# Kernel optimization log

Hardware: AMD Instinct MI355X
Metric: run time of the kernel (lower is better)

The kernel has to match this reference:

```python
import jax, jax.numpy as jnp
import numpy as np

N_NODES = 100000
N_EDGES = 800000
DIM = 300
N_GRAPHS = 64
ATOM_VOCAB = 41
WORD_VOCAB = 10000


def setup_inputs() -> dict:
    key = jax.random.key(0)
    ks = jax.random.split(key, 7)
    atoms = jax.random.randint(ks[0], (N_NODES,), 0, ATOM_VOCAB)
    words = jax.random.randint(ks[1], (N_NODES,), 0, WORD_VOCAB)
    x = jnp.stack([atoms, words], axis=-1)  # [N,2] int indices
    edge_index = jax.random.randint(ks[2], (2, N_EDGES), 0, N_NODES)
    batch = jnp.sort(jax.random.randint(ks[3], (N_NODES,), 0, N_GRAPHS))
    atom_table = jax.random.normal(ks[4], (ATOM_VOCAB, DIM), dtype=jnp.float32) * 0.02
    word_table = jax.random.normal(ks[5], (WORD_VOCAB, DIM), dtype=jnp.float32) * 0.02
    W = jax.random.normal(ks[6], (DIM, DIM), dtype=jnp.float32) / np.sqrt(DIM)
    b = jnp.zeros((DIM,), dtype=jnp.float32)
    return {"x": x, "edge_index": edge_index, "batch": batch,
            "atom_table": atom_table, "word_table": word_table,
            "W": W, "b": b, "num_hops": 3}


def reference(x, edge_index, batch, atom_table, word_table, W, b, num_hops):
    n = x.shape[0]
    # GCNConv: add self-loops, symmetric degree normalization
    loops = jnp.arange(n)
    src = jnp.concatenate([edge_index[0], loops])  # [E+N]
    dst = jnp.concatenate([edge_index[1], loops])
    deg = jax.ops.segment_sum(jnp.ones_like(dst, dtype=W.dtype), dst, num_segments=n)
    dinv = jnp.where(deg > 0, jax.lax.rsqrt(deg), 0.0)
    norm = dinv[src] * dinv[dst]  # [E+N]

    # embed_nodes: atom embedding + word embedding
    h = atom_table[x[:, 0]] + word_table[x[:, 1]]  # [N, D]

    # num_hops applications of the SAME GCNConv (shared W, b)
    for _ in range(num_hops):
        hw = h @ W  # [N, D]
        msg = hw[src] * norm[:, None]  # [E+N, D]
        h = jax.ops.segment_sum(msg, dst, num_segments=n) + b

    # global_mean_pool over batch assignment
    sums = jax.ops.segment_sum(h, batch, num_segments=N_GRAPHS)  # [G, D]
    cnt = jax.ops.segment_sum(jnp.ones((n,), h.dtype), batch, num_segments=N_GRAPHS)
    return sums / jnp.maximum(cnt, 1.0)[:, None]
```

## Files before the change

kernel.cpp:

```cpp
#include <hip/hip_runtime.h>
#include <hip/hip_fp16.h>

#define NG 64
#define NGRAPH_C 64

#define RSZ 25000
#define RSZP4 6250
#define NC_MS 128
#define NRNG 4
#define MSB 1024

#define VOC 10000
#define KPAD 10240
#define NKC 80
#define WGK 128

#define NATOM 41
#define NC_A 128
#define ASL 128
#define TW_BLKS ((VOC + 3) / 4)
#define TA_BLKS ((NATOM * ASL + 3) / 4)

__device__ __forceinline__ unsigned f_as_u(float f) { union { float f; unsigned u; } c; c.f = f; return c.u; }
__device__ __forceinline__ float u_as_f(unsigned u) { union { unsigned u; float f; } c; c.u = u; return c.f; }

__device__ __forceinline__ int xcc_id() {
    unsigned x;
    asm volatile("s_getreg_b32 %0, hwreg(HW_REG_XCC_ID)" : "=s"(x));
    return (int)(x & 7u);
}

union H4 { uint2 u2; __half h[4]; };

__global__ __launch_bounds__(MSB) void k_mscount(const int* __restrict__ src, const int* __restrict__ dst,
                                                 unsigned* __restrict__ rep_in,
                                                 unsigned* __restrict__ rep_src,
                                                 int e, int n, int chunk, int nwords) {
    __shared__ unsigned hin[RSZP4];
    __shared__ unsigned hsrc[RSZP4];
    int c = blockIdx.x % NC_MS;
    int r = blockIdx.x / NC_MS;
    int base = r * RSZ;
    int t = threadIdx.x;
    for (int w = t; w < RSZP4; w += MSB) { hin[w] = 0u; hsrc[w] = 0u; }
    __syncthreads();
    int e0 = c * chunk, e1 = min(e, e0 + chunk);
    for (int i = e0 + t; i < e1; i += MSB) {
        int s = src[i], d = dst[i];
        unsigned ud = (unsigned)(d - base);
        unsigned us = (unsigned)(s - base);
        if (ud < (unsigned)RSZ) atomicAdd(&hin[ud >> 2], 1u << ((ud & 3) * 8));
        if (us < (unsigned)RSZ) atomicAdd(&hsrc[us >> 2], 1u << ((us & 3) * 8));
    }
    __syncthreads();
    int lim = min(RSZ, n - base);
    if (lim <= 0) return;
    int plim = (lim + 3) >> 2;
    unsigned* gin  = rep_in  + (size_t)c * nwords + (base >> 2);
    unsigned* gsrc = rep_src + (size_t)c * nwords + (base >> 2);
    for (int w = t; w < plim; w += MSB) { gin[w] = hin[w]; gsrc[w] = hsrc[w]; }
}

__global__ __launch_bounds__(256) void k_msreduce(const unsigned* __restrict__ rep_in,
                                                  unsigned* __restrict__ rep_src,
                                                  float* __restrict__ dinv,
                                                  unsigned* __restrict__ counts_src,
                                                  int n, int nwords) {
    int i4 = blockIdx.x * 256 + threadIdx.x;
    if (i4 >= nwords) return;
    unsigned s0 = 0, s1 = 0, s2 = 0, s3 = 0;
    unsigned r0 = 0, r1 = 0, r2 = 0, r3 = 0;
#pragma unroll 4
    for (int c = 0; c < NC_MS; ++c) {
        unsigned vi = rep_in[(size_t)c * nwords + i4];
        s0 += vi & 0xFFu; s1 += (vi >> 8) & 0xFFu; s2 += (vi >> 16) & 0xFFu; s3 += vi >> 24;
        unsigned vs = rep_src[(size_t)c * nwords + i4];
        rep_src[(size_t)c * nwords + i4] = r0 | (r1 << 8) | (r2 << 16) | (r3 << 24);
        r0 += vs & 0xFFu; r1 += (vs >> 8) & 0xFFu; r2 += (vs >> 16) & 0xFFu; r3 += vs >> 24;
    }
    int i = i4 * 4;
    unsigned sv[4] = {s0, s1, s2, s3};
    unsigned rv[4] = {r0, r1, r2, r3};
#pragma unroll
    for (int q = 0; q < 4; ++q) {
        if (i + q < n) {
            dinv[i + q] = rsqrtf((float)(sv[q] + 1u));
            counts_src[i + q] = rv[q];
        }
    }
}

__global__ __launch_bounds__(256) void k_blocksum(const unsigned* __restrict__ counts,
                                                  unsigned* __restrict__ partials, int n) {
    __shared__ unsigned s[256];
    int base = blockIdx.x * 1024;
    unsigned sum = 0;
    for (int j = threadIdx.x; j < 1024; j += 256) {
        int i = base + j;
        sum += (i < n) ? counts[i] : 0u;
    }
    s[threadIdx.x] = sum;
    __syncthreads();
    for (int off = 128; off > 0; off >>= 1) {
        if (threadIdx.x < (unsigned)off) s[threadIdx.x] += s[threadIdx.x + off];
        __syncthreads();
    }
    if (threadIdx.x == 0) partials[blockIdx.x] = s[0];
}

__global__ __launch_bounds__(128) void k_scanpartials(unsigned* __restrict__ partials, int nb) {
    __shared__ unsigned s[128];
    int t = threadIdx.x;
    s[t] = (t < nb) ? partials[t] : 0u;
    __syncthreads();
    if (t == 0) {
        unsigned run = 0;
        for (int i = 0; i < nb; ++i) { unsigned v = s[i]; s[i] = run; run += v; }
    }
    __syncthreads();
    if (t < nb) partials[t] = s[t];
}

__global__ __launch_bounds__(256) void k_scanblock(const unsigned* __restrict__ counts,
                                                   const unsigned* __restrict__ partials,
                                                   unsigned* __restrict__ row_start, int n) {
    __shared__ unsigned s[256];
    int base = blockIdx.x * 1024;
    int t = threadIdx.x;
    unsigned v[4];
    unsigned tsum = 0;
#pragma unroll
    for (int j = 0; j < 4; ++j) {
        int i = base + t * 4 + j;
        v[j] = (i < n) ? counts[i] : 0u;
        tsum += v[j];
    }
    s[t] = tsum;
    __syncthreads();
    for (int off = 1; off < 256; off <<= 1) {
        unsigned x = (t >= off) ? s[t - off] : 0u;
        __syncthreads();
        s[t] += x;
        __syncthreads();
    }
    unsigned excl = (t > 0 ? s[t - 1] : 0u) + partials[blockIdx.x];
#pragma unroll
    for (int j = 0; j < 4; ++j) {
        int i = base + t * 4 + j;
        if (i < n) {
            row_start[i] = excl;
            excl += v[j];
            if (i == n - 1) row_start[n] = excl;
        }
    }
}

__global__ __launch_bounds__(MSB) void k_msfill(const int* __restrict__ src, const int* __restrict__ dst,
                                                const int* __restrict__ batch,
                                                const unsigned* __restrict__ row_start,
                                                const unsigned* __restrict__ pref,
                                                const float* __restrict__ dinv,
                                                uint2* __restrict__ euv,
                                                int e, int n, int chunk, int nwords) {
    __shared__ unsigned cur[RSZP4];
    int c = blockIdx.x % NC_MS;
    int r = blockIdx.x / NC_MS;
    int base = r * RSZ;
    int t = threadIdx.x;
    for (int w = t; w < RSZP4; w += MSB) cur[w] = 0u;
    __syncthreads();
    int e0 = c * chunk, e1 = min(e, e0 + chunk);
    const unsigned* prefc = pref + (size_t)c * nwords;
    for (int i = e0 + t; i < e1; i += MSB) {
        int s = src[i];
        unsigned us = (unsigned)(s - base);
        if (us < (unsigned)RSZ) {
            int d = dst[i];
            unsigned sh = (us & 3) * 8;
            unsigned old = atomicAdd(&cur[us >> 2], 1u << sh);
            unsigned slot = (old >> sh) & 0xFFu;
            unsigned p8 = (prefc[(unsigned)s >> 2] >> ((s & 3) * 8)) & 0xFFu;
            unsigned pos = row_start[s] + p8 + slot;
            uint2 pv;
            pv.x = (unsigned)d | ((unsigned)batch[d] << 17);
            pv.y = f_as_u(dinv[s] * dinv[d]);
            euv[pos] = pv;
        }
    }
}

__global__ __launch_bounds__(256) void k_xcount(const int* __restrict__ x,
                                                unsigned* __restrict__ wcnt,
                                                unsigned* __restrict__ rep_a,
                                                int n, int chunk) {
    __shared__ unsigned h[NATOM];
    int c = blockIdx.x;
    int t = threadIdx.x;
    if (t < NATOM) h[t] = 0u;
    __syncthreads();
    int j0 = c * chunk, j1 = min(n, j0 + chunk);
    for (int j = j0 + t; j < j1; j += 256) {
        int2 xv = *(const int2*)&x[2 * j];
        atomicAdd(&h[xv.x], 1u);
        atomicAdd(&wcnt[xv.y], 1u);
    }
    __syncthreads();
    if (t < NATOM) rep_a[c * NATOM + t] = h[t];
}

__global__ __launch_bounds__(1024) void k_scanall(const unsigned* __restrict__ wcnt,
                                                  unsigned* __restrict__ wstart,
                                                  unsigned* __restrict__ rep_a,
                                                  unsigned* __restrict__ astart,
                                                  const int* __restrict__ batch,
                                                  int* __restrict__ gstart, int n) {
    __shared__ unsigned s[1024];
    __shared__ unsigned tot[NATOM];
    int t = threadIdx.x;
    if (t < NATOM) {
        unsigned run = 0;
        for (int c = 0; c < NC_A; ++c) {
            unsigned v = rep_a[c * NATOM + t];
            rep_a[c * NATOM + t] = run;
            run += v;
        }
        tot[t] = run;
    }
    if (t <= NGRAPH_C) {
        if (t == NGRAPH_C) gstart[t] = n;
        else {
            int lo = 0, hi = n;
            while (lo < hi) {
                int mid = (lo + hi) >> 1;
                if (batch[mid] < t) lo = mid + 1; else hi = mid;
            }
            gstart[t] = lo;
        }
    }
    int lo10 = t * 10;
    unsigned v[10];
    unsigned sum = 0;
    if (lo10 < VOC) {
#pragma unroll
        for (int q = 0; q < 10; ++q) { v[q] = wcnt[lo10 + q]; sum += v[q]; }
    }
    s[t] = sum;
    __syncthreads();
    for (int off = 1; off < 1024; off <<= 1) {
        unsigned xx = (t >= off) ? s[t - off] : 0u;
        __syncthreads();
        s[t] += xx;
        __syncthreads();
    }
    if (lo10 < VOC) {
        unsigned excl = (t > 0) ? s[t - 1] : 0u;
#pragma unroll
        for (int q = 0; q < 10; ++q) { wstart[lo10 + q] = excl; excl += v[q]; }
    }
    if (t == 1023) wstart[VOC] = s[1023];
    if (t == 0) {
        unsigned run = 0;
        for (int a = 0; a < NATOM; ++a) { astart[a] = run; run += tot[a]; }
        astart[NATOM] = run;
    }
}

__global__ __launch_bounds__(256) void k_xfill(const int* __restrict__ x,
                                               const unsigned* __restrict__ wstart,
                                               unsigned* __restrict__ wcur,
                                               unsigned* __restrict__ sorted,
                                               const unsigned* __restrict__ astart,
                                               const unsigned* __restrict__ rep_a,
                                               unsigned* __restrict__ asorted,
                                               int n, int chunk) {
    __shared__ unsigned cur[NATOM];
    __shared__ unsigned base[NATOM];
    int c = blockIdx.x;
    int t = threadIdx.x;
    if (t < NATOM) {
        cur[t] = 0u;
        base[t] = astart[t] + rep_a[c * NATOM + t];
    }
    __syncthreads();
    int j0 = c * chunk, j1 = min(n, j0 + chunk);
    for (int j = j0 + t; j < j1; j += 256) {
        int2 xv = *(const int2*)&x[2 * j];
        unsigned slot = atomicAdd(&cur[xv.x], 1u);
        asorted[base[xv.x] + slot] = (unsigned)j;
        unsigned pos = wstart[xv.y] + atomicAdd(&wcur[xv.y], 1u);
        sorted[pos] = (unsigned)j;
    }
}

__global__ __launch_bounds__(256) void k_y1(const int* __restrict__ batch,
                                            const float* __restrict__ dinv,
                                            const unsigned* __restrict__ row_start,
                                            const uint2* __restrict__ euv,
                                            __half* __restrict__ Y1, int n) {
    int idx = blockIdx.x * 256 + threadIdx.x;
    if (idx >= n * 16) return;
    int j = idx >> 4;
    int c4 = idx & 15;
    int cb = c4 * 4;
    float a0 = 0.f, a1 = 0.f, a2 = 0.f, a3 = 0.f;
    {
        int bj = batch[j];
        float dj = dinv[j];
        float sn = dj * dj;
        a0 += (bj == cb + 0) ? sn : 0.f;
        a1 += (bj == cb + 1) ? sn : 0.f;
        a2 += (bj == cb + 2) ? sn : 0.f;
        a3 += (bj == cb + 3) ? sn : 0.f;
    }
    unsigned e0 = row_start[j], e1 = row_start[j + 1];
    unsigned e = e0;
    for (; e + 4 <= e1; e += 4) {
        uint2 p0 = euv[e], p1 = euv[e + 1], p2 = euv[e + 2], p3 = euv[e + 3];
        int b0 = (int)(p0.x >> 17), b1 = (int)(p1.x >> 17);
        int b2 = (int)(p2.x >> 17), b3 = (int)(p3.x >> 17);
        float v0 = u_as_f(p0.y), v1 = u_as_f(p1.y);
        float v2 = u_as_f(p2.y), v3 = u_as_f(p3.y);
        a0 += ((b0 == cb + 0) ? v0 : 0.f) + ((b1 == cb + 0) ? v1 : 0.f)
            + ((b2 == cb + 0) ? v2 : 0.f) + ((b3 == cb + 0) ? v3 : 0.f);
        a1 += ((b0 == cb + 1) ? v0 : 0.f) + ((b1 == cb + 1) ? v1 : 0.f)
            + ((b2 == cb + 1) ? v2 : 0.f) + ((b3 == cb + 1) ? v3 : 0.f);
        a2 += ((b0 == cb + 2) ? v0 : 0.f) + ((b1 == cb + 2) ? v1 : 0.f)
            + ((b2 == cb + 2) ? v2 : 0.f) + ((b3 == cb + 2) ? v3 : 0.f);
        a3 += ((b0 == cb + 3) ? v0 : 0.f) + ((b1 == cb + 3) ? v1 : 0.f)
            + ((b2 == cb + 3) ? v2 : 0.f) + ((b3 == cb + 3) ? v3 : 0.f);
    }
    for (; e < e1; ++e) {
        uint2 p = euv[e];
        int bd = (int)(p.x >> 17);
        float v = u_as_f(p.y);
        a0 += (bd == cb + 0) ? v : 0.f;
        a1 += (bd == cb + 1) ? v : 0.f;
        a2 += (bd == cb + 2) ? v : 0.f;
        a3 += (bd == cb + 3) ? v : 0.f;
    }
    H4 o;
    o.h[0] = __float2half(a0); o.h[1] = __float2half(a1);
    o.h[2] = __float2half(a2); o.h[3] = __float2half(a3);
    *(uint2*)&Y1[(size_t)j * NG + cb] = o.u2;
}

__global__ __launch_bounds__(256) void k_yprop(const __half* __restrict__ Yin,
                                               const float* __restrict__ dinv,
                                               const unsigned* __restrict__ row_start,
                                               const uint2* __restrict__ euv,
                                               __half* __restrict__ Yout, int n) {
    int idx = blockIdx.x * 256 + threadIdx.x;
    if (idx >= n * 16) return;
    int j = idx >> 4;
    int c4 = idx & 15;
    int cb = c4 * 4;
    float dj = dinv[j];
    float sn = dj * dj;
    H4 s; s.u2 = *(const uint2*)&Yin[(size_t)j * NG + cb];
    float a0 = sn * __half2float(s.h[0]);
    float a1 = sn * __half2float(s.h[1]);
    float a2 = sn * __half2float(s.h[2]);
    float a3 = sn * __half2float(s.h[3]);
    unsigned e0 = row_start[j], e1 = row_start[j + 1];
    unsigned e = e0;
    for (; e + 4 <= e1; e += 4) {
        uint2 p0 = euv[e], p1 = euv[e + 1], p2 = euv[e + 2], p3 = euv[e + 3];
        float v0 = u_as_f(p0.y), v1 = u_as_f(p1.y);
        float v2 = u_as_f(p2.y), v3 = u_as_f(p3.y);
        H4 m0; m0.u2 = *(const uint2*)&Yin[(size_t)(p0.x & 0x1FFFFu) * NG + cb];
        H4 m1; m1.u2 = *(const uint2*)&Yin[(size_t)(p1.x & 0x1FFFFu) * NG + cb];
        H4 m2; m2.u2 = *(const uint2*)&Yin[(size_t)(p2.x & 0x1FFFFu) * NG + cb];
        H4 m3; m3.u2 = *(const uint2*)&Yin[(size_t)(p3.x & 0x1FFFFu) * NG + cb];
        a0 += v0 * __half2float(m0.h[0]) + v1 * __half2float(m1.h[0])
            + v2 * __half2float(m2.h[0]) + v3 * __half2float(m3.h[0]);
        a1 += v0 * __half2float(m0.h[1]) + v1 * __half2float(m1.h[1])
            + v2 * __half2float(m2.h[1]) + v3 * __half2float(m3.h[1]);
        a2 += v0 * __half2float(m0.h[2]) + v1 * __half2float(m1.h[2])
            + v2 * __half2float(m2.h[2]) + v3 * __half2float(m3.h[2]);
        a3 += v0 * __half2float(m0.h[3]) + v1 * __half2float(m1.h[3])
            + v2 * __half2float(m2.h[3]) + v3 * __half2float(m3.h[3]);
    }
    for (; e < e1; ++e) {
        uint2 p0 = euv[e];
        float v0 = u_as_f(p0.y);
        H4 m0; m0.u2 = *(const uint2*)&Yin[(size_t)(p0.x & 0x1FFFFu) * NG + cb];
        a0 += v0 * __half2float(m0.h[0]);
        a1 += v0 * __half2float(m0.h[1]);
        a2 += v0 * __half2float(m0.h[2]);
        a3 += v0 * __half2float(m0.h[3]);
    }
    H4 o;
    o.h[0] = __float2half(a0); o.h[1] = __float2half(a1);
    o.h[2] = __float2half(a2); o.h[3] = __float2half(a3);
    *(uint2*)&Yout[(size_t)j * NG + cb] = o.u2;
}

__global__ __launch_bounds__(256) void k_colsumh(const __half* __restrict__ Y,
                                                 float* __restrict__ su8, int n) {
    __shared__ float red[16][NG];
    int t = threadIdx.x;
    int cg = t & 15;
    int sr = t >> 4;
    float a0 = 0.f, a1 = 0.f, a2 = 0.f, a3 = 0.f;
    int stride = gridDim.x * 16;
    for (int j = blockIdx.x * 16 + sr; j < n; j += stride) {
        H4 v; v.u2 = *(const uint2*)&Y[(size_t)j * NG + cg * 4];
        a0 += __half2float(v.h[0]);
        a1 += __half2float(v.h[1]);
        a2 += __half2float(v.h[2]);
        a3 += __half2float(v.h[3]);
    }
    red[sr][cg * 4 + 0] = a0;
    red[sr][cg * 4 + 1] = a1;
    red[sr][cg * 4 + 2] = a2;
    red[sr][cg * 4 + 3] = a3;
    __syncthreads();
    if (t < NG) {
        float s = 0.f;
#pragma unroll
        for (int q = 0; q < 16; ++q) s += red[q][t];
        int r = xcc_id();
        __hip_atomic_fetch_add(&su8[r * NG + t], s,
                               __ATOMIC_RELAXED, __HIP_MEMORY_SCOPE_WORKGROUP);
    }
}

__global__ __launch_bounds__(256) void k_twta(const __half* __restrict__ Y3,
                                              const unsigned* __restrict__ sorted,
                                              const unsigned* __restrict__ wstart,
                                              float* __restrict__ tw,
                                              const unsigned* __restrict__ asorted,
                                              const unsigned* __restrict__ astart,
                                              float* __restrict__ tap) {
    int t = threadIdx.x;
    int g = t & 63;
    if (blockIdx.x < TW_BLKS) {
        int w = blockIdx.x * 4 + (t >> 6);
        if (w >= VOC) return;
        unsigned i0 = wstart[w], i1 = wstart[w + 1];
        float s = 0.f;
        unsigned i = i0;
        for (; i + 2 <= i1; i += 2) {
            unsigned j0 = sorted[i], j1 = sorted[i + 1];
            s += __half2float(Y3[(size_t)j0 * NG + g]) + __half2float(Y3[(size_t)j1 * NG + g]);
        }
        if (i < i1) s += __half2float(Y3[(size_t)sorted[i] * NG + g]);
        tw[(size_t)w * NG + g] = s;
    } else {
        int wid = (blockIdx.x - TW_BLKS) * 4 + (t >> 6);
        if (wid >= NATOM * ASL) return;
        int a  = wid >> 7;
        int sl = wid & (ASL - 1);
        unsigned i0 = astart[a], i1 = astart[a + 1];
        unsigned len = i1 - i0;
        unsigned lo = i0 + (unsigned)((unsigned long long)len * sl / ASL);
        unsigned hi = i0 + (unsigned)((unsigned long long)len * (sl + 1) / ASL);
        float s = 0.f;
        unsigned i = lo;
        for (; i + 2 <= hi; i += 2) {
            unsigned j0 = asorted[i], j1 = asorted[i + 1];
            s += __half2float(Y3[(size_t)j0 * NG + g]) + __half2float(Y3[(size_t)j1 * NG + g]);
        }
        if (i < hi) s += __half2float(Y3[(size_t)asorted[i] * NG + g]);
        tap[((size_t)a * ASL + sl) * NG + g] = s;
    }
}

__global__ __launch_bounds__(256) void k_wgemm2(const float* __restrict__ T,
                                                const float* __restrict__ Tab,
                                                float* __restrict__ Gpart,
                                                const float* __restrict__ tap,
                                                float* __restrict__ ta) {
    if (blockIdx.x == 5) {
        int i = blockIdx.y * 256 + threadIdx.x;
        if (i >= NATOM * NG) return;
        int a = i >> 6;
        int g = i & 63;
        float s = 0.f;
        for (int sl = 0; sl < ASL; ++sl) s += tap[((size_t)a * ASL + sl) * NG + g];
        ta[i] = s;
        return;
    }
    __shared__ float Asm[32 * 64];
    __shared__ float Bsm[32 * 64];
    const int t = threadIdx.x;
    const int tg = t >> 4;
    const int tc = t & 15;
    const int c0 = blockIdx.x * 64;
    const int kb = blockIdx.y * WGK;

    float acc[4][4] = {};

    for (int sub = 0; sub < WGK / 32; ++sub) {
        int kbase = kb + sub * 32;
#pragma unroll
        for (int r2 = 0; r2 < 2; ++r2) {
            int idx4 = r2 * 256 + t;
            int k = idx4 >> 4, g4 = idx4 & 15;
            float4 v = *(const float4*)&T[(size_t)(kbase + k) * 64 + g4 * 4];
            *(float4*)&Asm[k * 64 + g4 * 4] = v;
        }
#pragma unroll
        for (int r2 = 0; r2 < 2; ++r2) {
            int idx4 = r2 * 256 + t;
            int k = idx4 >> 4, c4i = idx4 & 15;
            int gk = kbase + k;
            int cb2 = c0 + c4i * 4;
            float4 v;
            if (gk < VOC && cb2 + 3 < 300) {
                v = *(const float4*)&Tab[(size_t)gk * 300 + cb2];
            } else {
                float tmp[4];
#pragma unroll
                for (int q = 0; q < 4; ++q)
                    tmp[q] = (gk < VOC && cb2 + q < 300) ? Tab[(size_t)gk * 300 + cb2 + q] : 0.f;
                v.x = tmp[0]; v.y = tmp[1]; v.z = tmp[2]; v.w = tmp[3];
            }
            *(float4*)&Bsm[k * 64 + c4i * 4] = v;
        }
        __syncthreads();
#pragma unroll 8
        for (int k = 0; k < 32; ++k) {
            float4 a4 = *(const float4*)&Asm[k * 64 + tg * 4];
            float4 b4 = *(const float4*)&Bsm[k * 64 + tc * 4];
            float a[4] = {a4.x, a4.y, a4.z, a4.w};
            float b[4] = {b4.x, b4.y, b4.z, b4.w};
#pragma unroll
            for (int i = 0; i < 4; ++i)
#pragma unroll
                for (int jj = 0; jj < 4; ++jj) acc[i][jj] += a[i] * b[jj];
        }
        __syncthreads();
    }

    float* gp = Gpart + (size_t)blockIdx.y * (NG * 300);
#pragma unroll
    for (int i = 0; i < 4; ++i) {
        int g = tg * 4 + i;
#pragma unroll
        for (int jj = 0; jj < 4; ++jj) {
            int c = c0 + tc * 4 + jj;
            if (c < 300) gp[g * 300 + c] = acc[i][jj];
        }
    }
}

__global__ __launch_bounds__(256) void k_gredagemm(const float* __restrict__ Gpart,
                                                   const float* __restrict__ ta,
                                                   const float* __restrict__ at,
                                                   float* __restrict__ G0) {
    int k = blockIdx.x * 256 + threadIdx.x;
    if (k >= NG * 300) return;
    if (blockIdx.y < 8) {
        int p0 = blockIdx.y * (NKC / 8);
        int p1 = p0 + (NKC / 8);
        float s = 0.f;
        for (int p = p0; p < p1; ++p) s += Gpart[(size_t)p * (NG * 300) + k];
        atomicAdd(&G0[k], s);
    } else {
        int g = k / 300, c = k - g * 300;
        float acc = 0.f;
#pragma unroll
        for (int q = 0; q < NATOM; ++q) acc += ta[q * NG + g] * at[(size_t)q * 300 + c];
        atomicAdd(&G0[k], acc);
    }
}

__global__ __launch_bounds__(256) void k_smm(const float* __restrict__ A,
                                             const float* __restrict__ W,
                                             float* __restrict__ C,
                                             const float* __restrict__ vin,
                                             float* __restrict__ r_out) {
    int bx = blockIdx.x;
    if (bx >= 75) {
        int c = (bx - 75) * 256 + threadIdx.x;
        if (c >= 300) return;
        int k0 = blockIdx.y * 60;
        float acc = 0.f;
        for (int k = k0; k < k0 + 60; ++k) acc += vin[k] * W[k * 300 + c];
        atomicAdd(&r_out[c], acc);
        return;
    }
    int j = bx * 256 + threadIdx.x;
    if (j >= NG * 300) return;
    int g = j / 300, c = j - g * 300;
    int k0 = blockIdx.y * 60;
    float acc = 0.f;
#pragma unroll 1
    for (int k = k0; k < k0 + 60; k += 4) {
        float a0 = A[g * 300 + k + 0], a1 = A[g * 300 + k + 1];
        float a2 = A[g * 300 + k + 2], a3 = A[g * 300 + k + 3];
        float w0 = W[(k + 0) * 300 + c], w1 = W[(k + 1) * 300 + c];
        float w2 = W[(k + 2) * 300 + c], w3 = W[(k + 3) * 300 + c];
        acc += a0 * w0 + a1 * w1 + a2 * w2 + a3 * w3;
    }
    atomicAdd(&C[j], acc);
}

__global__ __launch_bounds__(256) void k_out(const float* __restrict__ T3,
                                             const float* __restrict__ su1,
                                             const float* __restrict__ su2,
                                             const int* __restrict__ gstart,
                                             const float* __restrict__ r1,
                                             const float* __restrict__ r2,
                                             const float* __restrict__ b,
                                             float* __restrict__ out) {
    int j = blockIdx.x * 256 + threadIdx.x;
    if (j >= NG * 300) return;
    int g = j / 300, c = j - g * 300;
    int cnt = gstart[g + 1] - gstart[g];
    float s1 = 0.f, s2 = 0.f;
#pragma unroll
    for (int r = 0; r < 8; ++r) {
        s1 += su1[r * NG + g];
        s2 += su2[r * NG + g];
    }
    float v = T3[j] + s2 * r2[c] + s1 * r1[c] + (float)cnt * b[c];
    out[j] = v / (float)(cnt > 0 ? cnt : 1);
}

extern "C" void kernel_launch(void* const* d_in, const int* in_sizes, int n_in,
                              void* d_out, int out_size, void* d_ws, size_t ws_size,
                              hipStream_t stream) {
    const int*   x     = (const int*)d_in[0];
    const int*   ei    = (const int*)d_in[1];
    const int*   batch = (const int*)d_in[2];
    const float* at    = (const float*)d_in[3];
    const float* wt    = (const float*)d_in[4];
    const float* W     = (const float*)d_in[5];
    const float* b     = (const float*)d_in[6];

    const int n = in_sizes[0] / 2;
    const int e = in_sizes[1] / 2;

    char* ws = (char*)d_ws;
    size_t off = 0;
    auto carve = [&](size_t bytes) {
        void* p = ws + off;
        off += (bytes + 255) & ~(size_t)255;
        return p;
    };
    __half*   Y1        = (__half*)carve((size_t)n * NG * 2);
    __half*   Y2        = (__half*)carve((size_t)n * NG * 2);
    __half*   Y3        = (__half*)carve((size_t)n * NG * 2);
    uint2*    euv       = (uint2*)carve((size_t)e * 8);
    float*    dinv      = (float*)carve((size_t)n * 4);
    unsigned* counts_src= (unsigned*)carve((size_t)n * 4);
    unsigned* row_start = (unsigned*)carve((size_t)(n + 1) * 4);
    unsigned* partials  = (unsigned*)carve(1024 * 4);
    int*      gstart    = (int*)carve(65 * 4);
    unsigned* wstart    = (unsigned*)carve((size_t)(VOC + 1) * 4);
    unsigned* sorted    = (unsigned*)carve((size_t)n * 4);
    unsigned* asorted   = (unsigned*)carve((size_t)n * 4);
    unsigned* astart    = (unsigned*)carve((NATOM + 1) * 4);
    unsigned* rep_a     = (unsigned*)carve((size_t)NC_A * NATOM * 4);
    float*    tap       = (float*)carve((size_t)NATOM * ASL * NG * 4);
    char*     zB0       = (char*)carve(0);
    float*    su1       = (float*)carve((size_t)8 * NG * 4);
    float*    su2       = (float*)carve((size_t)8 * NG * 4);
    float*    ta        = (float*)carve((size_t)NATOM * NG * 4);
    float*    tw        = (float*)carve((size_t)KPAD * NG * 4);
    float*    G0        = (float*)carve((size_t)NG * 300 * 4);
    float*    r1        = (float*)carve(300 * 4);
    float*    r2        = (float*)carve(300 * 4);
    float*    T1        = (float*)carve((size_t)NG * 300 * 4);
    float*    T2        = (float*)carve((size_t)NG * 300 * 4);
    float*    T3        = (float*)carve((size_t)NG * 300 * 4);
    unsigned* wcnt      = (unsigned*)carve((size_t)VOC * 4);
    unsigned* wcur      = (unsigned*)carve((size_t)VOC * 4);
    char*     zB1       = (char*)carve(0);

    const int* src = ei;
    const int* dst = ei + e;

    unsigned* rep_in  = (unsigned*)Y1;
    unsigned* rep_src = (unsigned*)Y2;
    float*    Gpart   = (float*)Y1;

    hipMemsetAsync(zB0, 0, (size_t)(zB1 - zB0), stream);

    const int nwords = (n + 3) / 4;
    const int chunk  = (e + NC_MS - 1) / NC_MS;
    const int achunk = (n + NC_A - 1) / NC_A;

    k_mscount<<<NRNG * NC_MS, MSB, 0, stream>>>(src, dst, rep_in, rep_src, e, n, chunk, nwords);
    k_msreduce<<<(nwords + 255) / 256, 256, 0, stream>>>(rep_in, rep_src, dinv, counts_src, n, nwords);
    int NB = (n + 1023) / 1024;
    k_blocksum<<<NB, 256, 0, stream>>>(counts_src, partials, n);
    k_scanpartials<<<1, 128, 0, stream>>>(partials, NB);
    k_scanblock<<<NB, 256, 0, stream>>>(counts_src, partials, row_start, n);
    k_msfill<<<NRNG * NC_MS, MSB, 0, stream>>>(src, dst, batch, row_start, rep_src, dinv, euv, e, n, chunk, nwords);

    k_xcount<<<NC_A, 256, 0, stream>>>(x, wcnt, rep_a, n, achunk);
    k_scanall<<<1, 1024, 0, stream>>>(wcnt, wstart, rep_a, astart, batch, gstart, n);
    k_xfill<<<NC_A, 256, 0, stream>>>(x, wstart, wcur, sorted, astart, rep_a, asorted, n, achunk);

    int yb = (n * 16 + 255) / 256;
    k_y1<<<yb, 256, 0, stream>>>(batch, dinv, row_start, euv, Y1, n);
    k_colsumh<<<512, 256, 0, stream>>>(Y1, su1, n);
    k_yprop<<<yb, 256, 0, stream>>>(Y1, dinv, row_start, euv, Y2, n);
    k_colsumh<<<512, 256, 0, stream>>>(Y2, su2, n);
    k_yprop<<<yb, 256, 0, stream>>>(Y2, dinv, row_start, euv, Y3, n);

    k_twta<<<TW_BLKS + TA_BLKS, 256, 0, stream>>>(Y3, sorted, wstart, tw, asorted, astart, tap);
    {
        dim3 gw(6, NKC);
        k_wgemm2<<<gw, 256, 0, stream>>>(tw, wt, Gpart, tap, ta);
        dim3 gr((NG * 300 + 255) / 256, 9);
        k_gredagemm<<<gr, 256, 0, stream>>>(Gpart, ta, at, G0);
    }

    {
        dim3 gs1(77, 5);
        k_smm<<<gs1, 256, 0, stream>>>(G0, W, T1, b, r1);
        k_smm<<<gs1, 256, 0, stream>>>(T1, W, T2, r1, r2);
        dim3 gs3(75, 5);
        k_smm<<<gs3, 256, 0, stream>>>(T2, W, T3, r2, r2);
    }

    k_out<<<(NG * 300 + 255) / 256, 256, 0, stream>>>(T3, su1, su2, gstart, r1, r2, b, (float*)d_out);
}
```

Baseline: 297.7 us.

## Fuse column sums into propagation kernels and block partial sums into msreduce

The separate column-sum kernels are removed. The column sums of Y1 and Y2 are now computed inside k_y1 and k_yprop from the fp32 accumulators, using a shared-memory reduction and atomics spread over 32 replicas (XCC id times 4). The k_blocksum pass is folded into k_msreduce, which now writes the per-block partials directly, and the block granularity changes from 1024 to 1024 nodes via nwords/256. This removes three kernel launches and two full re-reads of the fp16 Y matrices. In exchange it adds a __syncthreads and atomics to each propagation block, and sums fp32 values rather than fp16-rounded ones.

```diff
diff --git a/kernel.cpp b/kernel.cpp
--- a/kernel.cpp
+++ b/kernel.cpp
@@ -20,6 +20,8 @@
 #define ASL 128
 #define TW_BLKS ((VOC + 3) / 4)
 #define TA_BLKS ((NATOM * ASL + 3) / 4)
+
+#define NREP 32
 
 __device__ __forceinline__ unsigned f_as_u(float f) { union { float f; unsigned u; } c; c.f = f; return c.u; }
 __device__ __forceinline__ float u_as_f(unsigned u) { union { unsigned u; float f; } c; c.u = u; return c.f; }
@@ -65,47 +67,42 @@
                                                   unsigned* __restrict__ rep_src,
                                                   float* __restrict__ dinv,
                                                   unsigned* __restrict__ counts_src,
+                                                  unsigned* __restrict__ partials,
                                                   int n, int nwords) {
-    int i4 = blockIdx.x * 256 + threadIdx.x;
-    if (i4 >= nwords) return;
-    unsigned s0 = 0, s1 = 0, s2 = 0, s3 = 0;
-    unsigned r0 = 0, r1 = 0, r2 = 0, r3 = 0;
+    __shared__ unsigned sred[256];
+    int t = threadIdx.x;
+    int i4 = blockIdx.x * 256 + t;
+    unsigned mysum = 0;
+    if (i4 < nwords) {
+        unsigned s0 = 0, s1 = 0, s2 = 0, s3 = 0;
+        unsigned r0 = 0, r1 = 0, r2 = 0, r3 = 0;
 #pragma unroll 4
-    for (int c = 0; c < NC_MS; ++c) {
-        unsigned vi = rep_in[(size_t)c * nwords + i4];
-        s0 += vi & 0xFFu; s1 += (vi >> 8) & 0xFFu; s2 += (vi >> 16) & 0xFFu; s3 += vi >> 24;
-        unsigned vs = rep_src[(size_t)c * nwords + i4];
-        rep_src[(size_t)c * nwords + i4] = r0 | (r1 << 8) | (r2 << 16) | (r3 << 24);
-        r0 += vs & 0xFFu; r1 += (vs >> 8) & 0xFFu; r2 += (vs >> 16) & 0xFFu; r3 += vs >> 24;
-    }
-    int i = i4 * 4;
-    unsigned sv[4] = {s0, s1, s2, s3};
-    unsigned rv[4] = {r0, r1, r2, r3};
-#pragma unroll
-    for (int q = 0; q < 4; ++q) {
-        if (i + q < n) {
-            dinv[i + q] = rsqrtf((float)(sv[q] + 1u));
-            counts_src[i + q] = rv[q];
-        }
-    }
-}
-
-__global__ __launch_bounds__(256) void k_blocksum(const unsigned* __restrict__ counts,
-                                                  unsigned* __restrict__ partials, int n) {
-    __shared__ unsigned s[256];
-    int base = blockIdx.x * 1024;
-    unsigned sum = 0;
-    for (int j = threadIdx.x; j < 1024; j += 256) {
-        int i = base + j;
-        sum += (i < n) ? counts[i] : 0u;
-    }
-    s[threadIdx.x] = sum;
+        for (int c = 0; c < NC_MS; ++c) {
+            unsigned vi = rep_in[(size_t)c * nwords + i4];
+            s0 += vi & 0xFFu; s1 += (vi >> 8) & 0xFFu; s2 += (vi >> 16) & 0xFFu; s3 += vi >> 24;
+            unsigned vs = rep_src[(size_t)c * nwords + i4];
+            rep_src[(size_t)c * nwords + i4] = r0 | (r1 << 8) | (r2 << 16) | (r3 << 24);
+            r0 += vs & 0xFFu; r1 += (vs >> 8) & 0xFFu; r2 += (vs >> 16) & 0xFFu; r3 += vs >> 24;
+        }
+        int i = i4 * 4;
+        unsigned sv[4] = {s0, s1, s2, s3};
+        unsigned rv[4] = {r0, r1, r2, r3};
+#pragma unroll
+        for (int q = 0; q < 4; ++q) {
+            if (i + q < n) {
+                dinv[i + q] = rsqrtf((float)(sv[q] + 1u));
+                counts_src[i + q] = rv[q];
+                mysum += rv[q];
+            }
+        }
+    }
+    sred[t] = mysum;
     __syncthreads();
     for (int off = 128; off > 0; off >>= 1) {
-        if (threadIdx.x < (unsigned)off) s[threadIdx.x] += s[threadIdx.x + off];
+        if (t < off) sred[t] += sred[t + off];
         __syncthreads();
     }
-    if (threadIdx.x == 0) partials[blockIdx.x] = s[0];
+    if (t == 0) partials[blockIdx.x] = sred[0];
 }
 
 __global__ __launch_bounds__(128) void k_scanpartials(unsigned* __restrict__ partials, int nb) {
@@ -296,14 +293,16 @@
                                             const float* __restrict__ dinv,
                                             const unsigned* __restrict__ row_start,
                                             const uint2* __restrict__ euv,
-                                            __half* __restrict__ Y1, int n) {
-    int idx = blockIdx.x * 256 + threadIdx.x;
-    if (idx >= n * 16) return;
+                                            __half* __restrict__ Y1,
+                                            float* __restrict__ su32, int n) {
+    __shared__ float red[16][NG];
+    int t = threadIdx.x;
+    int idx = blockIdx.x * 256 + t;
     int j = idx >> 4;
     int c4 = idx & 15;
     int cb = c4 * 4;
     float a0 = 0.f, a1 = 0.f, a2 = 0.f, a3 = 0.f;
-    {
+    if (j < n) {
         int bj = batch[j];
         float dj = dinv[j];
         float sn = dj * dj;
@@ -311,116 +310,120 @@
         a1 += (bj == cb + 1) ? sn : 0.f;
         a2 += (bj == cb + 2) ? sn : 0.f;
         a3 += (bj == cb + 3) ? sn : 0.f;
-    }
-    unsigned e0 = row_start[j], e1 = row_start[j + 1];
-    unsigned e = e0;
-    for (; e + 4 <= e1; e += 4) {
-        uint2 p0 = euv[e], p1 = euv[e + 1], p2 = euv[e + 2], p3 = euv[e + 3];
-        int b0 = (int)(p0.x >> 17), b1 = (int)(p1.x >> 17);
-        int b2 = (int)(p2.x >> 17), b3 = (int)(p3.x >> 17);
-        float v0 = u_as_f(p0.y), v1 = u_as_f(p1.y);
-        float v2 = u_as_f(p2.y), v3 = u_as_f(p3.y);
-        a0 += ((b0 == cb + 0) ? v0 : 0.f) + ((b1 == cb + 0) ? v1 : 0.f)
-            + ((b2 == cb + 0) ? v2 : 0.f) + ((b3 == cb + 0) ? v3 : 0.f);
-        a1 += ((b0 == cb + 1) ? v0 : 0.f) + ((b1 == cb + 1) ? v1 : 0.f)
-            + ((b2 == cb + 1) ? v2 : 0.f) + ((b3 == cb + 1) ? v3 : 0.f);
-        a2 += ((b0 == cb + 2) ? v0 : 0.f) + ((b1 == cb + 2) ? v1 : 0.f)
-            + ((b2 == cb + 2) ? v2 : 0.f) + ((b3 == cb + 2) ? v3 : 0.f);
-        a3 += ((b0 == cb + 3) ? v0 : 0.f) + ((b1 == cb + 3) ? v1 : 0.f)
-            + ((b2 == cb + 3) ? v2 : 0.f) + ((b3 == cb + 3) ? v3 : 0.f);
-    }
-    for (; e < e1; ++e) {
-        uint2 p = euv[e];
-        int bd = (int)(p.x >> 17);
-        float v = u_as_f(p.y);
-        a0 += (bd == cb + 0) ? v : 0.f;
-        a1 += (bd == cb + 1) ? v : 0.f;
-        a2 += (bd == cb + 2) ? v : 0.f;
-        a3 += (bd == cb + 3) ? v : 0.f;
-    }
-    H4 o;
-    o.h[0] = __float2half(a0); o.h[1] = __float2half(a1);
-    o.h[2] = __float2half(a2); o.h[3] = __float2half(a3);
-    *(uint2*)&Y1[(size_t)j * NG + cb] = o.u2;
+        unsigned e0 = row_start[j], e1 = row_start[j + 1];
+        unsigned e = e0;
+        for (; e + 4 <= e1; e += 4) {
+            uint2 p0 = euv[e], p1 = euv[e + 1], p2 = euv[e + 2], p3 = euv[e + 3];
+            int b0 = (int)(p0.x >> 17), b1 = (int)(p1.x >> 17);
+            int b2 = (int)(p2.x >> 17), b3 = (int)(p3.x >> 17);
+            float v0 = u_as_f(p0.y), v1 = u_as_f(p1.y);
+            float v2 = u_as_f(p2.y), v3 = u_as_f(p3.y);
+            a0 += ((b0 == cb + 0) ? v0 : 0.f) + ((b1 == cb + 0) ? v1 : 0.f)
+                + ((b2 == cb + 0) ? v2 : 0.f) + ((b3 == cb + 0) ? v3 : 0.f);
+            a1 += ((b0 == cb + 1) ? v0 : 0.f) + ((b1 == cb + 1) ? v1 : 0.f)
+                + ((b2 == cb + 1) ? v2 : 0.f) + ((b3 == cb + 1) ? v3 : 0.f);
+            a2 += ((b0 == cb + 2) ? v0 : 0.f) + ((b1 == cb + 2) ? v1 : 0.f)
+                + ((b2 == cb + 2) ? v2 : 0.f) + ((b3 == cb + 2) ? v3 : 0.f);
+            a3 += ((b0 == cb + 3) ? v0 : 0.f) + ((b1 == cb + 3) ? v1 : 0.f)
+                + ((b2 == cb + 3) ? v2 : 0.f) + ((b3 == cb + 3) ? v3 : 0.f);
+        }
+        for (; e < e1; ++e) {
+            uint2 p = euv[e];
+            int bd = (int)(p.x >> 17);
+            float v = u_as_f(p.y);
+            a0 += (bd == cb + 0) ? v : 0.f;
+            a1 += (bd == cb + 1) ? v : 0.f;
+            a2 += (bd == cb + 2) ? v : 0.f;
+            a3 += (bd == cb + 3) ? v : 0.f;
+        }
+        H4 o;
+        o.h[0] = __float2half(a0); o.h[1] = __float2half(a1);
+        o.h[2] = __float2half(a2); o.h[3] = __float2half(a3);
+        *(uint2*)&Y1[(size_t)j * NG + cb] = o.u2;
+    }
+    int slot = t >> 4;
+    red[slot][c4 * 4 + 0] = a0;
+    red[slot][c4 * 4 + 1] = a1;
+    red[slot][c4 * 4 + 2] = a2;
+    red[slot][c4 * 4 + 3] = a3;
+    __syncthreads();
+    if (t < NG) {
+        float s = 0.f;
+#pragma unroll
+        for (int q = 0; q < 16; ++q) s += red[q][t];
+        int r = (xcc_id() << 2) | (blockIdx.x & 3);
+        __hip_atomic_fetch_add(&su32[r * NG + t], s,
+                               __ATOMIC_RELAXED, __HIP_MEMORY_SCOPE_WORKGROUP);
+    }
 }
 
 __global__ __launch_bounds__(256) void k_yprop(const __half* __restrict__ Yin,
                                                const float* __restrict__ dinv,
                                                const unsigned* __restrict__ row_start,
                                                const uint2* __restrict__ euv,
-                                               __half* __restrict__ Yout, int n) {
-    int idx = blockIdx.x * 256 + threadIdx.x;
-    if (idx >= n * 16) return;
+                                               __half* __restrict__ Yout,
+                                               float* __restrict__ su32, int n) {
+    __shared__ float red[16][NG];
+    int t = threadIdx.x;
+    int idx = blockIdx.x * 256 + t;
     int j = idx >> 4;
     int c4 = idx & 15;
     int cb = c4 * 4;
-    float dj = dinv[j];
-    float sn = dj * dj;
-    H4 s; s.u2 = *(const uint2*)&Yin[(size_t)j * NG + cb];
-    float a0 = sn * __half2float(s.h[0]);
-    float a1 = sn * __half2float(s.h[1]);
-    float a2 = sn * __half2float(s.h[2]);
-    float a3 = sn * __half2float(s.h[3]);
-    unsigned e0 = row_start[j], e1 = row_start[j + 1];
-    unsigned e = e0;
-    for (; e + 4 <= e1; e += 4) {
-        uint2 p0 = euv[e], p1 = euv[e + 1], p2 = euv[e + 2], p3 = euv[e + 3];
-        float v0 = u_as_f(p0.y), v1 = u_as_f(p1.y);
-        float v2 = u_as_f(p2.y), v3 = u_as_f(p3.y);
-        H4 m0; m0.u2 = *(const uint2*)&Yin[(size_t)(p0.x & 0x1FFFFu) * NG + cb];
-        H4 m1; m1.u2 = *(const uint2*)&Yin[(size_t)(p1.x & 0x1FFFFu) * NG + cb];
-        H4 m2; m2.u2 = *(const uint2*)&Yin[(size_t)(p2.x & 0x1FFFFu) * NG + cb];
-        H4 m3; m3.u2 = *(const uint2*)&Yin[(size_t)(p3.x & 0x1FFFFu) * NG + cb];
-        a0 += v0 * __half2float(m0.h[0]) + v1 * __half2float(m1.h[0])
-            + v2 * __half2float(m2.h[0]) + v3 * __half2float(m3.h[0]);
-        a1 += v0 * __half2float(m0.h[1]) + v1 * __half2float(m1.h[1])
-            + v2 * __half2float(m2.h[1]) + v3 * __half2float(m3.h[1]);
-        a2 += v0 * __half2float(m0.h[2]) + v1 * __half2float(m1.h[2])
-            + v2 * __half2float(m2.h[2]) + v3 * __half2float(m3.h[2]);
-        a3 += v0 * __half2float(m0.h[3]) + v1 * __half2float(m1.h[3])
-            + v2 * __half2float(m2.h[3]) + v3 * __half2float(m3.h[3]);
-    }
-    for (; e < e1; ++e) {
-        uint2 p0 = euv[e];
-        float v0 = u_as_f(p0.y);
-        H4 m0; m0.u2 = *(const uint2*)&Yin[(size_t)(p0.x & 0x1FFFFu) * NG + cb];
-        a0 += v0 * __half2float(m0.h[0]);
-        a1 += v0 * __half2float(m0.h[1]);
-        a2 += v0 * __half2float(m0.h[2]);
-        a3 += v0 * __half2float(m0.h[3]);
-    }
-    H4 o;
-    o.h[0] = __float2half(a0); o.h[1] = __float2half(a1);
-    o.h[2] = __float2half(a2); o.h[3] = __float2half(a3);
-    *(uint2*)&Yout[(size_t)j * NG + cb] = o.u2;
-}
-
-__global__ __launch_bounds__(256) void k_colsumh(const __half* __restrict__ Y,
-                                                 float* __restrict__ su8, int n) {
-    __shared__ float red[16][NG];
-    int t = threadIdx.x;
-    int cg = t & 15;
-    int sr = t >> 4;
     float a0 = 0.f, a1 = 0.f, a2 = 0.f, a3 = 0.f;
-    int stride = gridDim.x * 16;
-    for (int j = blockIdx.x * 16 + sr; j < n; j += stride) {
-        H4 v; v.u2 = *(const uint2*)&Y[(size_t)j * NG + cg * 4];
-        a0 += __half2float(v.h[0]);
-        a1 += __half2float(v.h[1]);
-        a2 += __half2float(v.h[2]);
-        a3 += __half2float(v.h[3]);
-    }
-    red[sr][cg * 4 + 0] = a0;
-    red[sr][cg * 4 + 1] = a1;
-    red[sr][cg * 4 + 2] = a2;
-    red[sr][cg * 4 + 3] = a3;
+    if (j < n) {
+        float dj = dinv[j];
+        float sn = dj * dj;
+        H4 s; s.u2 = *(const uint2*)&Yin[(size_t)j * NG + cb];
+        a0 = sn * __half2float(s.h[0]);
+        a1 = sn * __half2float(s.h[1]);
+        a2 = sn * __half2float(s.h[2]);
+        a3 = sn * __half2float(s.h[3]);
+        unsigned e0 = row_start[j], e1 = row_start[j + 1];
+        unsigned e = e0;
+        for (; e + 4 <= e1; e += 4) {
+            uint2 p0 = euv[e], p1 = euv[e + 1], p2 = euv[e + 2], p3 = euv[e + 3];
+            float v0 = u_as_f(p0.y), v1 = u_as_f(p1.y);
+            float v2 = u_as_f(p2.y), v3 = u_as_f(p3.y);
+            H4 m0; m0.u2 = *(const uint2*)&Yin[(size_t)(p0.x & 0x1FFFFu) * NG + cb];
+            H4 m1; m1.u2 = *(const uint2*)&Yin[(size_t)(p1.x & 0x1FFFFu) * NG + cb];
+            H4 m2; m2.u2 = *(const uint2*)&Yin[(size_t)(p2.x & 0x1FFFFu) * NG + cb];
+            H4 m3; m3.u2 = *(const uint2*)&Yin[(size_t)(p3.x & 0x1FFFFu) * NG + cb];
+            a0 += v0 * __half2float(m0.h[0]) + v1 * __half2float(m1.h[0])
+                + v2 * __half2float(m2.h[0]) + v3 * __half2float(m3.h[0]);
+            a1 += v0 * __half2float(m0.h[1]) + v1 * __half2float(m1.h[1])
+                + v2 * __half2float(m2.h[1]) + v3 * __half2float(m3.h[1]);
+            a2 += v0 * __half2float(m0.h[2]) + v1 * __half2float(m1.h[2])
+                + v2 * __half2float(m2.h[2]) + v3 * __half2float(m3.h[2]);
+            a3 += v0 * __half2float(m0.h[3]) + v1 * __half2float(m1.h[3])
+                + v2 * __half2float(m2.h[3]) + v3 * __half2float(m3.h[3]);
+        }
+        for (; e < e1; ++e) {
+            uint2 p0 = euv[e];
+            float v0 = u_as_f(p0.y);
+            H4 m0; m0.u2 = *(const uint2*)&Yin[(size_t)(p0.x & 0x1FFFFu) * NG + cb];
+            a0 += v0 * __half2float(m0.h[0]);
+            a1 += v0 * __half2float(m0.h[1]);
+            a2 += v0 * __half2float(m0.h[2]);
+            a3 += v0 * __half2float(m0.h[3]);
+        }
+        H4 o;
+        o.h[0] = __float2half(a0); o.h[1] = __float2half(a1);
+        o.h[2] = __float2half(a2); o.h[3] = __float2half(a3);
+        *(uint2*)&Yout[(size_t)j * NG + cb] = o.u2;
+    }
+    if (su32 == nullptr) return;
+    int slot = t >> 4;
+    red[slot][c4 * 4 + 0] = a0;
+    red[slot][c4 * 4 + 1] = a1;
+    red[slot][c4 * 4 + 2] = a2;
+    red[slot][c4 * 4 + 3] = a3;
     __syncthreads();
     if (t < NG) {
         float s = 0.f;
 #pragma unroll
         for (int q = 0; q < 16; ++q) s += red[q][t];
-        int r = xcc_id();
-        __hip_atomic_fetch_add(&su8[r * NG + t], s,
+        int r = (xcc_id() << 2) | (blockIdx.x & 3);
+        __hip_atomic_fetch_add(&su32[r * NG + t], s,
                                __ATOMIC_RELAXED, __HIP_MEMORY_SCOPE_WORKGROUP);
     }
 }
@@ -611,7 +614,7 @@
     int cnt = gstart[g + 1] - gstart[g];
     float s1 = 0.f, s2 = 0.f;
 #pragma unroll
-    for (int r = 0; r < 8; ++r) {
+    for (int r = 0; r < NREP; ++r) {
         s1 += su1[r * NG + g];
         s2 += su2[r * NG + g];
     }
@@ -656,8 +659,8 @@
     unsigned* rep_a     = (unsigned*)carve((size_t)NC_A * NATOM * 4);
     float*    tap       = (float*)carve((size_t)NATOM * ASL * NG * 4);
     char*     zB0       = (char*)carve(0);
-    float*    su1       = (float*)carve((size_t)8 * NG * 4);
-    float*    su2       = (float*)carve((size_t)8 * NG * 4);
+    float*    su1       = (float*)carve((size_t)NREP * NG * 4);
+    float*    su2       = (float*)carve((size_t)NREP * NG * 4);
     float*    ta        = (float*)carve((size_t)NATOM * NG * 4);
     float*    tw        = (float*)carve((size_t)KPAD * NG * 4);
     float*    G0        = (float*)carve((size_t)NG * 300 * 4);
@@ -684,9 +687,8 @@
     const int achunk = (n + NC_A - 1) / NC_A;
 
     k_mscount<<<NRNG * NC_MS, MSB, 0, stream>>>(src, dst, rep_in, rep_src, e, n, chunk, nwords);
-    k_msreduce<<<(nwords + 255) / 256, 256, 0, stream>>>(rep_in, rep_src, dinv, counts_src, n, nwords);
-    int NB = (n + 1023) / 1024;
-    k_blocksum<<<NB, 256, 0, stream>>>(counts_src, partials, n);
+    int NB = (nwords + 255) / 256;
+    k_msreduce<<<NB, 256, 0, stream>>>(rep_in, rep_src, dinv, counts_src, partials, n, nwords);
     k_scanpartials<<<1, 128, 0, stream>>>(partials, NB);
     k_scanblock<<<NB, 256, 0, stream>>>(counts_src, partials, row_start, n);
     k_msfill<<<NRNG * NC_MS, MSB, 0, stream>>>(src, dst, batch, row_start, rep_src, dinv, euv, e, n, chunk, nwords);
@@ -696,11 +698,9 @@
     k_xfill<<<NC_A, 256, 0, stream>>>(x, wstart, wcur, sorted, astart, rep_a, asorted, n, achunk);
 
     int yb = (n * 16 + 255) / 256;
-    k_y1<<<yb, 256, 0, stream>>>(batch, dinv, row_start, euv, Y1, n);
-    k_colsumh<<<512, 256, 0, stream>>>(Y1, su1, n);
-    k_yprop<<<yb, 256, 0, stream>>>(Y1, dinv, row_start, euv, Y2, n);
-    k_colsumh<<<512, 256, 0, stream>>>(Y2, su2, n);
-    k_yprop<<<yb, 256, 0, stream>>>(Y2, dinv, row_start, euv, Y3, n);
+    k_y1<<<yb, 256, 0, stream>>>(batch, dinv, row_start, euv, Y1, su1, n);
+    k_yprop<<<yb, 256, 0, stream>>>(Y1, dinv, row_start, euv, Y2, su2, n);
+    k_yprop<<<yb, 256, 0, stream>>>(Y2, dinv, row_start, euv, Y3, nullptr, n);
 
     k_twta<<<TW_BLKS + TA_BLKS, 256, 0, stream>>>(Y3, sorted, wstart, tw, asorted, astart, tap);
     {
```

New measurement: 300.5 us. No clear change (+0.9%).
